# Kernel tuning notes

Hardware: AMD Instinct MI355X
Metric: run time of the kernel (lower is better)

## Reference

```python
import jax, jax.numpy as jnp
import numpy as np

N_NODES = 60000
IN_CH = 128
HID = 32
ACT_DIM = 6
N_EDGES = 600000


def setup_inputs() -> dict:
    key = jax.random.key(0)
    ks = jax.random.split(key, 10)
    state = jax.random.normal(ks[0], (N_NODES, IN_CH), dtype=jnp.float32)
    edge_index = jax.random.randint(ks[1], (2, N_EDGES), 0, N_NODES, dtype=jnp.int64)
    s_g = 1.0 / np.sqrt(IN_CH)
    s_h = 1.0 / np.sqrt(HID)
    Wg = jax.random.uniform(ks[2], (IN_CH, IN_CH), jnp.float32, -s_g, s_g)
    bg = jax.random.uniform(ks[3], (IN_CH,), jnp.float32, -s_g, s_g)
    W1 = jax.random.uniform(ks[4], (IN_CH, HID), jnp.float32, -s_g, s_g)
    b1 = jax.random.uniform(ks[5], (HID,), jnp.float32, -s_g, s_g)
    W2 = jax.random.uniform(ks[6], (HID, HID), jnp.float32, -s_h, s_h)
    b2 = jax.random.uniform(ks[7], (HID,), jnp.float32, -s_h, s_h)
    W3 = jax.random.uniform(ks[8], (HID, 1), jnp.float32, -s_h, s_h)
    b3 = jax.random.uniform(ks[9], (1,), jnp.float32, -s_h, s_h)
    return {"state": state, "Wg": Wg, "bg": bg, "W1": W1, "b1": b1,
            "W2": W2, "b2": b2, "W3": W3, "b3": b3, "edge_index": edge_index}


def reference(state, Wg, bg, W1, b1, W2, b2, W3, b3, edge_index):
    N = state.shape[0]
    # GCNConv: add self-loops, symmetric degree normalization
    loop = jnp.arange(N, dtype=edge_index.dtype)
    src = jnp.concatenate([edge_index[0], loop])
    dst = jnp.concatenate([edge_index[1], loop])
    deg = jax.ops.segment_sum(jnp.ones_like(dst, dtype=state.dtype), dst, num_segments=N)
    dinv = jax.lax.rsqrt(deg)  # deg >= 1 thanks to self-loops
    norm = dinv[src] * dinv[dst]  # [E+N]
    h = state @ Wg  # [N, C]
    agg = jax.ops.segment_sum(h[src] * norm[:, None], dst, num_segments=N) + bg
    out = jax.nn.relu(agg)
    x = (out + state).reshape(-1, ACT_DIM, IN_CH)  # [B, 6, C]
    x = jax.nn.leaky_relu(x @ W1 + b1)
    x = jax.nn.leaky_relu(x @ W2 + b2)
    conc = jax.nn.softplus(x @ W3 + b3)[..., 0]  # [B, 6]
    # deterministic, mode==0
    action = conc / (conc.sum() + 1e-20)
    return action
```

## Files before the change

### kernel.cpp

```cpp
#include <hip/hip_runtime.h>
#include <hip/hip_bf16.h>
#include <math.h>

#define N_NODES 60000
#define IN_CH   128
#define HID     32
#define N_EDGES 600000
#define CAP     48

#define WS_CNT    0
#define WS_SUM    60000
#define WS_BUCKET 60008
#define WS_HS     2940032
#define WS_X      10620032

typedef float  v4f __attribute__((ext_vector_type(4)));
typedef short  v8s __attribute__((ext_vector_type(8)));

static __device__ inline short f2bf(float f) {
    __hip_bfloat16 h = __float2bfloat16(f);
    union { __hip_bfloat16 h; short s; } u; u.h = h; return u.s;
}

__global__ void k_hist(const int* __restrict__ eidx, int* __restrict__ cnt,
                       int* __restrict__ bucket) {
    int i = blockIdx.x * blockDim.x + threadIdx.x;
    if (i >= N_EDGES) return;
    int s = eidx[i];
    int d = eidx[N_EDGES + i];
    int slot = atomicAdd(&cnt[d], 1);
    if (slot < CAP) bucket[d * CAP + slot] = s;
}

__launch_bounds__(256)
__global__ void k_gemm(const float* __restrict__ state, const float* __restrict__ Wg,
                       const int* __restrict__ cnt, unsigned short* __restrict__ hs) {
    __shared__ __align__(16) short Bs[128 * 136];
    const int t = threadIdx.x;
    for (int idx = t; idx < 128 * 128; idx += 256) {
        int k = idx >> 7, n = idx & 127;
        Bs[n * 136 + k] = f2bf(Wg[idx]);
    }
    __syncthreads();

    const int w = t >> 6, lane = t & 63;
    const int quad = lane >> 4, m = lane & 15;
    const int rowBase = blockIdx.x * 64;
    int arow = rowBase + w * 16 + m;
    if (arow > N_NODES - 1) arow = N_NODES - 1;

    v8s a[4];
    const float4* sp = (const float4*)(state + (size_t)arow * 128);
#pragma unroll
    for (int q = 0; q < 4; ++q) {
        float4 v0 = sp[q * 8 + quad * 2];
        float4 v1 = sp[q * 8 + quad * 2 + 1];
        v8s af;
        af[0] = f2bf(v0.x); af[1] = f2bf(v0.y); af[2] = f2bf(v0.z); af[3] = f2bf(v0.w);
        af[4] = f2bf(v1.x); af[5] = f2bf(v1.y); af[6] = f2bf(v1.z); af[7] = f2bf(v1.w);
        a[q] = af;
    }

    v4f acc[8];
#pragma unroll
    for (int tt = 0; tt < 8; ++tt) acc[tt] = (v4f)0.f;

#pragma unroll
    for (int tt = 0; tt < 8; ++tt) {
        const short* bp = &Bs[(tt * 16 + m) * 136];
#pragma unroll
        for (int q = 0; q < 4; ++q) {
            v8s b = *(const v8s*)(bp + q * 32 + quad * 8);
            acc[tt] = __builtin_amdgcn_mfma_f32_16x16x32_bf16(a[q], b, acc[tt], 0, 0, 0);
        }
    }

    float dinv[4];
#pragma unroll
    for (int r = 0; r < 4; ++r) {
        int rr = rowBase + w * 16 + quad * 4 + r;
        dinv[r] = (rr < N_NODES) ? rsqrtf((float)cnt[rr] + 1.0f) : 0.f;
    }
#pragma unroll
    for (int tt = 0; tt < 8; ++tt) {
#pragma unroll
        for (int r = 0; r < 4; ++r) {
            int rr = rowBase + w * 16 + quad * 4 + r;
            if (rr < N_NODES)
                hs[(size_t)rr * 128 + tt * 16 + m] = (unsigned short)f2bf(acc[tt][r] * dinv[r]);
        }
    }
}

__launch_bounds__(256)
__global__ void k_gather(const unsigned short* __restrict__ hs, const float* __restrict__ state,
                         const int* __restrict__ cnt, const int* __restrict__ bucket,
                         const float* __restrict__ bg, float* __restrict__ x) {
    const int wave = threadIdx.x >> 6, lane = threadIdx.x & 63;
    const int row = blockIdx.x * 4 + wave;
    if (row >= N_NODES) return;
    const int ci = cnt[row];
    const float dinv = rsqrtf((float)ci + 1.0f);
    const int nb = ci < CAP ? ci : CAP;

    int slot = (lane < nb) ? bucket[row * CAP + lane] : 0;

    const unsigned int* hp = (const unsigned int*)hs;
    float ax, ay;
    {
        unsigned int u = hp[row * 64 + lane];
        ax = __uint_as_float(u << 16);
        ay = __uint_as_float(u & 0xffff0000u);
    }
    int s = 0;
    for (; s + 8 <= nb; s += 8) {
        unsigned int u0 = hp[__shfl(slot, s + 0, 64) * 64 + lane];
        unsigned int u1 = hp[__shfl(slot, s + 1, 64) * 64 + lane];
        unsigned int u2 = hp[__shfl(slot, s + 2, 64) * 64 + lane];
        unsigned int u3 = hp[__shfl(slot, s + 3, 64) * 64 + lane];
        unsigned int u4 = hp[__shfl(slot, s + 4, 64) * 64 + lane];
        unsigned int u5 = hp[__shfl(slot, s + 5, 64) * 64 + lane];
        unsigned int u6 = hp[__shfl(slot, s + 6, 64) * 64 + lane];
        unsigned int u7 = hp[__shfl(slot, s + 7, 64) * 64 + lane];
        ax += __uint_as_float(u0 << 16) + __uint_as_float(u1 << 16)
            + __uint_as_float(u2 << 16) + __uint_as_float(u3 << 16)
            + __uint_as_float(u4 << 16) + __uint_as_float(u5 << 16)
            + __uint_as_float(u6 << 16) + __uint_as_float(u7 << 16);
        ay += __uint_as_float(u0 & 0xffff0000u) + __uint_as_float(u1 & 0xffff0000u)
            + __uint_as_float(u2 & 0xffff0000u) + __uint_as_float(u3 & 0xffff0000u)
            + __uint_as_float(u4 & 0xffff0000u) + __uint_as_float(u5 & 0xffff0000u)
            + __uint_as_float(u6 & 0xffff0000u) + __uint_as_float(u7 & 0xffff0000u);
    }
    for (; s + 4 <= nb; s += 4) {
        unsigned int u0 = hp[__shfl(slot, s + 0, 64) * 64 + lane];
        unsigned int u1 = hp[__shfl(slot, s + 1, 64) * 64 + lane];
        unsigned int u2 = hp[__shfl(slot, s + 2, 64) * 64 + lane];
        unsigned int u3 = hp[__shfl(slot, s + 3, 64) * 64 + lane];
        ax += __uint_as_float(u0 << 16) + __uint_as_float(u1 << 16)
            + __uint_as_float(u2 << 16) + __uint_as_float(u3 << 16);
        ay += __uint_as_float(u0 & 0xffff0000u) + __uint_as_float(u1 & 0xffff0000u)
            + __uint_as_float(u2 & 0xffff0000u) + __uint_as_float(u3 & 0xffff0000u);
    }
    for (; s < nb; ++s) {
        unsigned int u = hp[__shfl(slot, s, 64) * 64 + lane];
        ax += __uint_as_float(u << 16);
        ay += __uint_as_float(u & 0xffff0000u);
    }
    float2 bgv = ((const float2*)bg)[lane];
    float2 st  = ((const float2*)state)[row * 64 + lane];
    float2 o;
    o.x = fmaxf(fmaf(dinv, ax, bgv.x), 0.f) + st.x;
    o.y = fmaxf(fmaf(dinv, ay, bgv.y), 0.f) + st.y;
    ((float2*)x)[row * 64 + lane] = o;
}

__launch_bounds__(256)
__global__ void k_mlp(const float* __restrict__ x,
                      const float* __restrict__ W1, const float* __restrict__ b1,
                      const float* __restrict__ W2, const float* __restrict__ b2,
                      const float* __restrict__ W3, const float* __restrict__ b3,
                      float* __restrict__ out, float* __restrict__ sum) {
    __shared__ float4 W1s[128 * 8];
    __shared__ float4 W2s[32 * 8];
    __shared__ float  W3s[32];
    __shared__ float  wred[4];
    const int t = threadIdx.x;
#pragma unroll
    for (int i = 0; i < 4; ++i) W1s[t + 256 * i] = ((const float4*)W1)[t + 256 * i];
    W2s[t] = ((const float4*)W2)[t];
    if (t < 32) W3s[t] = W3[t];
    __syncthreads();

    const int r = blockIdx.x * 256 + t;
    float sp = 0.f;
    if (r < N_NODES) {
        float h1[32];
#pragma unroll
        for (int j = 0; j < 32; ++j) h1[j] = b1[j];
        const float4* xr = (const float4*)(x + (size_t)r * 128);
#pragma unroll 4
        for (int k4 = 0; k4 < 32; ++k4) {
            float4 xv = xr[k4];
            float xa[4] = {xv.x, xv.y, xv.z, xv.w};
#pragma unroll
            for (int kk = 0; kk < 4; ++kk) {
                float xk = xa[kk];
#pragma unroll
                for (int j4 = 0; j4 < 8; ++j4) {
                    float4 w = W1s[(k4 * 4 + kk) * 8 + j4];
                    h1[j4 * 4 + 0] = fmaf(xk, w.x, h1[j4 * 4 + 0]);
                    h1[j4 * 4 + 1] = fmaf(xk, w.y, h1[j4 * 4 + 1]);
                    h1[j4 * 4 + 2] = fmaf(xk, w.z, h1[j4 * 4 + 2]);
                    h1[j4 * 4 + 3] = fmaf(xk, w.w, h1[j4 * 4 + 3]);
                }
            }
        }
        float z1[32];
#pragma unroll
        for (int j = 0; j < 32; ++j) z1[j] = h1[j] > 0.f ? h1[j] : 0.01f * h1[j];
        float h2[32];
#pragma unroll
        for (int j = 0; j < 32; ++j) h2[j] = b2[j];
#pragma unroll
        for (int k = 0; k < 32; ++k) {
            float zk = z1[k];
#pragma unroll
            for (int j4 = 0; j4 < 8; ++j4) {
                float4 w = W2s[k * 8 + j4];
                h2[j4 * 4 + 0] = fmaf(zk, w.x, h2[j4 * 4 + 0]);
                h2[j4 * 4 + 1] = fmaf(zk, w.y, h2[j4 * 4 + 1]);
                h2[j4 * 4 + 2] = fmaf(zk, w.z, h2[j4 * 4 + 2]);
                h2[j4 * 4 + 3] = fmaf(zk, w.w, h2[j4 * 4 + 3]);
            }
        }
        float a3 = b3[0];
#pragma unroll
        for (int j = 0; j < 32; ++j) {
            float z2 = h2[j] > 0.f ? h2[j] : 0.01f * h2[j];
            a3 = fmaf(z2, W3s[j], a3);
        }
        sp = fmaxf(a3, 0.f) + log1pf(expf(-fabsf(a3)));
        out[r] = sp;
    }
    float p = sp;
#pragma unroll
    for (int off = 32; off >= 1; off >>= 1) p += __shfl_xor(p, off, 64);
    if ((t & 63) == 0) wred[t >> 6] = p;
    __syncthreads();
    if (t == 0) atomicAdd(sum, (wred[0] + wred[1]) + (wred[2] + wred[3]));
}

__global__ void k_norm(const float* __restrict__ sum, float* __restrict__ out) {
    int i = blockIdx.x * blockDim.x + threadIdx.x;
    if (i < N_NODES) out[i] = out[i] / (*sum + 1e-20f);
}

extern "C" void kernel_launch(void* const* d_in, const int* in_sizes, int n_in,
                              void* d_out, int out_size, void* d_ws, size_t ws_size,
                              hipStream_t stream) {
    const float* state = (const float*)d_in[0];
    const float* Wg    = (const float*)d_in[1];
    const float* bg    = (const float*)d_in[2];
    const float* W1    = (const float*)d_in[3];
    const float* b1    = (const float*)d_in[4];
    const float* W2    = (const float*)d_in[5];
    const float* b2    = (const float*)d_in[6];
    const float* W3    = (const float*)d_in[7];
    const float* b3    = (const float*)d_in[8];
    const int*   eidx  = (const int*)d_in[9];
    float* out = (float*)d_out;

    int*   wi = (int*)d_ws;
    float* wf = (float*)d_ws;
    int*   cnt    = wi + WS_CNT;
    float* sum    = wf + WS_SUM;
    int*   bucket = wi + WS_BUCKET;
    unsigned short* hs = (unsigned short*)(wf + WS_HS);
    float* x      = wf + WS_X;

    hipMemsetAsync(cnt, 0, 60001 * sizeof(int), stream);
    k_hist<<<(N_EDGES + 255) / 256, 256, 0, stream>>>(eidx, cnt, bucket);
    k_gemm<<<(N_NODES + 63) / 64, 256, 0, stream>>>(state, Wg, cnt, hs);
    k_gather<<<(N_NODES + 3) / 4, 256, 0, stream>>>(hs, state, cnt, bucket, bg, x);
    k_mlp<<<(N_NODES + 255) / 256, 256, 0, stream>>>(x, W1, b1, W2, b2, W3, b3, out, sum);
    k_norm<<<(N_NODES + 255) / 256, 256, 0, stream>>>(sum, out);
}
```

Measured before the change: 191.9 us.

## Fuse histogram and GEMM into one launch, store x as bf16

Merges the edge-bucketing histogram and the dense GEMM into one kernel whose blocks are split 2:5 between GEMM and histogram work, so both run concurrently. To remove the GEMM's dependency on degree counts, the source-side dinv scaling moves into the gather, which loads each neighbour's count and applies it per edge. The intermediate x is written as packed bf16 instead of fp32, halving its traffic into the MLP. The final normalization is vectorized to float4. This adds extra count loads and shuffles in the gather and more bf16 rounding error.

```diff
diff --git a/kernel.cpp b/kernel.cpp
--- a/kernel.cpp
+++ b/kernel.cpp
@@ -21,22 +21,32 @@
     __hip_bfloat16 h = __float2bfloat16(f);
     union { __hip_bfloat16 h; short s; } u; u.h = h; return u.s;
 }
-
-__global__ void k_hist(const int* __restrict__ eidx, int* __restrict__ cnt,
-                       int* __restrict__ bucket) {
-    int i = blockIdx.x * blockDim.x + threadIdx.x;
-    if (i >= N_EDGES) return;
-    int s = eidx[i];
-    int d = eidx[N_EDGES + i];
-    int slot = atomicAdd(&cnt[d], 1);
-    if (slot < CAP) bucket[d * CAP + slot] = s;
-}
+static __device__ inline float bflo(unsigned int u) { return __uint_as_float(u << 16); }
+static __device__ inline float bfhi(unsigned int u) { return __uint_as_float(u & 0xffff0000u); }
 
 __launch_bounds__(256)
-__global__ void k_gemm(const float* __restrict__ state, const float* __restrict__ Wg,
-                       const int* __restrict__ cnt, unsigned short* __restrict__ hs) {
+__global__ void k_fat(const float* __restrict__ state, const float* __restrict__ Wg,
+                      const int* __restrict__ eidx, int* __restrict__ cnt,
+                      int* __restrict__ bucket, unsigned short* __restrict__ hs) {
     __shared__ __align__(16) short Bs[128 * 136];
+    const int bid = blockIdx.x;
+    const int r7 = bid % 7, q7 = bid / 7;
     const int t = threadIdx.x;
+
+    if (r7 >= 2) {
+        const int hb = q7 * 5 + (r7 - 2);
+        const int i = hb * 256 + t;
+        if (i < N_EDGES) {
+            int s = eidx[i];
+            int d = eidx[N_EDGES + i];
+            int slot = atomicAdd(&cnt[d], 1);
+            if (slot < CAP) bucket[d * CAP + slot] = s;
+        }
+        return;
+    }
+
+    const int gb = q7 * 2 + r7;
+
     for (int idx = t; idx < 128 * 128; idx += 256) {
         int k = idx >> 7, n = idx & 127;
         Bs[n * 136 + k] = f2bf(Wg[idx]);
@@ -45,7 +55,7 @@
 
     const int w = t >> 6, lane = t & 63;
     const int quad = lane >> 4, m = lane & 15;
-    const int rowBase = blockIdx.x * 64;
+    const int rowBase = gb * 64;
     int arow = rowBase + w * 16 + m;
     if (arow > N_NODES - 1) arow = N_NODES - 1;
 
@@ -75,19 +85,13 @@
         }
     }
 
-    float dinv[4];
-#pragma unroll
-    for (int r = 0; r < 4; ++r) {
-        int rr = rowBase + w * 16 + quad * 4 + r;
-        dinv[r] = (rr < N_NODES) ? rsqrtf((float)cnt[rr] + 1.0f) : 0.f;
-    }
 #pragma unroll
     for (int tt = 0; tt < 8; ++tt) {
 #pragma unroll
         for (int r = 0; r < 4; ++r) {
             int rr = rowBase + w * 16 + quad * 4 + r;
             if (rr < N_NODES)
-                hs[(size_t)rr * 128 + tt * 16 + m] = (unsigned short)f2bf(acc[tt][r] * dinv[r]);
+                hs[(size_t)rr * 128 + tt * 16 + m] = (unsigned short)f2bf(acc[tt][r]);
         }
     }
 }
@@ -95,7 +99,7 @@
 __launch_bounds__(256)
 __global__ void k_gather(const unsigned short* __restrict__ hs, const float* __restrict__ state,
                          const int* __restrict__ cnt, const int* __restrict__ bucket,
-                         const float* __restrict__ bg, float* __restrict__ x) {
+                         const float* __restrict__ bg, unsigned int* __restrict__ xb) {
     const int wave = threadIdx.x >> 6, lane = threadIdx.x & 63;
     const int row = blockIdx.x * 4 + wave;
     if (row >= N_NODES) return;
@@ -103,59 +107,78 @@
     const float dinv = rsqrtf((float)ci + 1.0f);
     const int nb = ci < CAP ? ci : CAP;
 
-    int slot = (lane < nb) ? bucket[row * CAP + lane] : 0;
+    int slot = 0; float dv = 0.f;
+    if (lane < nb) {
+        slot = bucket[row * CAP + lane];
+        dv = rsqrtf((float)cnt[slot] + 1.0f);
+    }
 
     const unsigned int* hp = (const unsigned int*)hs;
     float ax, ay;
     {
-        unsigned int u = hp[row * 64 + lane];
-        ax = __uint_as_float(u << 16);
-        ay = __uint_as_float(u & 0xffff0000u);
+        unsigned int u = hp[(size_t)row * 64 + lane];
+        ax = bflo(u) * dinv;
+        ay = bfhi(u) * dinv;
     }
     int s = 0;
     for (; s + 8 <= nb; s += 8) {
-        unsigned int u0 = hp[__shfl(slot, s + 0, 64) * 64 + lane];
-        unsigned int u1 = hp[__shfl(slot, s + 1, 64) * 64 + lane];
-        unsigned int u2 = hp[__shfl(slot, s + 2, 64) * 64 + lane];
-        unsigned int u3 = hp[__shfl(slot, s + 3, 64) * 64 + lane];
-        unsigned int u4 = hp[__shfl(slot, s + 4, 64) * 64 + lane];
-        unsigned int u5 = hp[__shfl(slot, s + 5, 64) * 64 + lane];
-        unsigned int u6 = hp[__shfl(slot, s + 6, 64) * 64 + lane];
-        unsigned int u7 = hp[__shfl(slot, s + 7, 64) * 64 + lane];
-        ax += __uint_as_float(u0 << 16) + __uint_as_float(u1 << 16)
-            + __uint_as_float(u2 << 16) + __uint_as_float(u3 << 16)
-            + __uint_as_float(u4 << 16) + __uint_as_float(u5 << 16)
-            + __uint_as_float(u6 << 16) + __uint_as_float(u7 << 16);
-        ay += __uint_as_float(u0 & 0xffff0000u) + __uint_as_float(u1 & 0xffff0000u)
-            + __uint_as_float(u2 & 0xffff0000u) + __uint_as_float(u3 & 0xffff0000u)
-            + __uint_as_float(u4 & 0xffff0000u) + __uint_as_float(u5 & 0xffff0000u)
-            + __uint_as_float(u6 & 0xffff0000u) + __uint_as_float(u7 & 0xffff0000u);
+        int s0 = __shfl(slot, s + 0, 64), s1 = __shfl(slot, s + 1, 64);
+        int s2 = __shfl(slot, s + 2, 64), s3 = __shfl(slot, s + 3, 64);
+        int s4 = __shfl(slot, s + 4, 64), s5 = __shfl(slot, s + 5, 64);
+        int s6 = __shfl(slot, s + 6, 64), s7 = __shfl(slot, s + 7, 64);
+        float d0 = __shfl(dv, s + 0, 64), d1 = __shfl(dv, s + 1, 64);
+        float d2 = __shfl(dv, s + 2, 64), d3 = __shfl(dv, s + 3, 64);
+        float d4 = __shfl(dv, s + 4, 64), d5 = __shfl(dv, s + 5, 64);
+        float d6 = __shfl(dv, s + 6, 64), d7 = __shfl(dv, s + 7, 64);
+        unsigned int u0 = hp[(size_t)s0 * 64 + lane];
+        unsigned int u1 = hp[(size_t)s1 * 64 + lane];
+        unsigned int u2 = hp[(size_t)s2 * 64 + lane];
+        unsigned int u3 = hp[(size_t)s3 * 64 + lane];
+        unsigned int u4 = hp[(size_t)s4 * 64 + lane];
+        unsigned int u5 = hp[(size_t)s5 * 64 + lane];
+        unsigned int u6 = hp[(size_t)s6 * 64 + lane];
+        unsigned int u7 = hp[(size_t)s7 * 64 + lane];
+        ax = fmaf(d0, bflo(u0), ax); ay = fmaf(d0, bfhi(u0), ay);
+        ax = fmaf(d1, bflo(u1), ax); ay = fmaf(d1, bfhi(u1), ay);
+        ax = fmaf(d2, bflo(u2), ax); ay = fmaf(d2, bfhi(u2), ay);
+        ax = fmaf(d3, bflo(u3), ax); ay = fmaf(d3, bfhi(u3), ay);
+        ax = fmaf(d4, bflo(u4), ax); ay = fmaf(d4, bfhi(u4), ay);
+        ax = fmaf(d5, bflo(u5), ax); ay = fmaf(d5, bfhi(u5), ay);
+        ax = fmaf(d6, bflo(u6), ax); ay = fmaf(d6, bfhi(u6), ay);
+        ax = fmaf(d7, bflo(u7), ax); ay = fmaf(d7, bfhi(u7), ay);
     }
     for (; s + 4 <= nb; s += 4) {
-        unsigned int u0 = hp[__shfl(slot, s + 0, 64) * 64 + lane];
-        unsigned int u1 = hp[__shfl(slot, s + 1, 64) * 64 + lane];
-        unsigned int u2 = hp[__shfl(slot, s + 2, 64) * 64 + lane];
-        unsigned int u3 = hp[__shfl(slot, s + 3, 64) * 64 + lane];
-        ax += __uint_as_float(u0 << 16) + __uint_as_float(u1 << 16)
-            + __uint_as_float(u2 << 16) + __uint_as_float(u3 << 16);
-        ay += __uint_as_float(u0 & 0xffff0000u) + __uint_as_float(u1 & 0xffff0000u)
-            + __uint_as_float(u2 & 0xffff0000u) + __uint_as_float(u3 & 0xffff0000u);
+        int s0 = __shfl(slot, s + 0, 64), s1 = __shfl(slot, s + 1, 64);
+        int s2 = __shfl(slot, s + 2, 64), s3 = __shfl(slot, s + 3, 64);
+        float d0 = __shfl(dv, s + 0, 64), d1 = __shfl(dv, s + 1, 64);
+        float d2 = __shfl(dv, s + 2, 64), d3 = __shfl(dv, s + 3, 64);
+        unsigned int u0 = hp[(size_t)s0 * 64 + lane];
+        unsigned int u1 = hp[(size_t)s1 * 64 + lane];
+        unsigned int u2 = hp[(size_t)s2 * 64 + lane];
+        unsigned int u3 = hp[(size_t)s3 * 64 + lane];
+        ax = fmaf(d0, bflo(u0), ax); ay = fmaf(d0, bfhi(u0), ay);
+        ax = fmaf(d1, bflo(u1), ax); ay = fmaf(d1, bfhi(u1), ay);
+        ax = fmaf(d2, bflo(u2), ax); ay = fmaf(d2, bfhi(u2), ay);
+        ax = fmaf(d3, bflo(u3), ax); ay = fmaf(d3, bfhi(u3), ay);
     }
     for (; s < nb; ++s) {
-        unsigned int u = hp[__shfl(slot, s, 64) * 64 + lane];
-        ax += __uint_as_float(u << 16);
-        ay += __uint_as_float(u & 0xffff0000u);
+        int s0 = __shfl(slot, s, 64);
+        float d0 = __shfl(dv, s, 64);
+        unsigned int u = hp[(size_t)s0 * 64 + lane];
+        ax = fmaf(d0, bflo(u), ax);
+        ay = fmaf(d0, bfhi(u), ay);
     }
     float2 bgv = ((const float2*)bg)[lane];
-    float2 st  = ((const float2*)state)[row * 64 + lane];
-    float2 o;
-    o.x = fmaxf(fmaf(dinv, ax, bgv.x), 0.f) + st.x;
-    o.y = fmaxf(fmaf(dinv, ay, bgv.y), 0.f) + st.y;
-    ((float2*)x)[row * 64 + lane] = o;
+    float2 st  = ((const float2*)state)[(size_t)row * 64 + lane];
+    float ox = fmaxf(fmaf(dinv, ax, bgv.x), 0.f) + st.x;
+    float oy = fmaxf(fmaf(dinv, ay, bgv.y), 0.f) + st.y;
+    unsigned int pack = ((unsigned int)(unsigned short)f2bf(oy) << 16)
+                      | ((unsigned int)(unsigned short)f2bf(ox));
+    xb[(size_t)row * 64 + lane] = pack;
 }
 
 __launch_bounds__(256)
-__global__ void k_mlp(const float* __restrict__ x,
+__global__ void k_mlp(const unsigned int* __restrict__ xb,
                       const float* __restrict__ W1, const float* __restrict__ b1,
                       const float* __restrict__ W2, const float* __restrict__ b2,
                       const float* __restrict__ W3, const float* __restrict__ b3,
@@ -177,17 +200,17 @@
         float h1[32];
 #pragma unroll
         for (int j = 0; j < 32; ++j) h1[j] = b1[j];
-        const float4* xr = (const float4*)(x + (size_t)r * 128);
-#pragma unroll 4
-        for (int k4 = 0; k4 < 32; ++k4) {
-            float4 xv = xr[k4];
-            float xa[4] = {xv.x, xv.y, xv.z, xv.w};
-#pragma unroll
-            for (int kk = 0; kk < 4; ++kk) {
-                float xk = xa[kk];
+        const v8s* xr = (const v8s*)(xb + (size_t)r * 64);
+#pragma unroll 2
+        for (int k8 = 0; k8 < 16; ++k8) {
+            v8s xv = xr[k8];
+#pragma unroll
+            for (int jj = 0; jj < 8; ++jj) {
+                float xk = __uint_as_float(((unsigned int)(unsigned short)xv[jj]) << 16);
+                const int k = k8 * 8 + jj;
 #pragma unroll
                 for (int j4 = 0; j4 < 8; ++j4) {
-                    float4 w = W1s[(k4 * 4 + kk) * 8 + j4];
+                    float4 w = W1s[k * 8 + j4];
                     h1[j4 * 4 + 0] = fmaf(xk, w.x, h1[j4 * 4 + 0]);
                     h1[j4 * 4 + 1] = fmaf(xk, w.y, h1[j4 * 4 + 1]);
                     h1[j4 * 4 + 2] = fmaf(xk, w.z, h1[j4 * 4 + 2]);
@@ -232,7 +255,13 @@
 
 __global__ void k_norm(const float* __restrict__ sum, float* __restrict__ out) {
     int i = blockIdx.x * blockDim.x + threadIdx.x;
-    if (i < N_NODES) out[i] = out[i] / (*sum + 1e-20f);
+    if (i < N_NODES / 4) {
+        float inv = 1.0f / (*sum + 1e-20f);
+        float4* o4 = (float4*)out;
+        float4 v = o4[i];
+        v.x *= inv; v.y *= inv; v.z *= inv; v.w *= inv;
+        o4[i] = v;
+    }
 }
 
 extern "C" void kernel_launch(void* const* d_in, const int* in_sizes, int n_in,
@@ -256,12 +285,12 @@
     float* sum    = wf + WS_SUM;
     int*   bucket = wi + WS_BUCKET;
     unsigned short* hs = (unsigned short*)(wf + WS_HS);
-    float* x      = wf + WS_X;
+    unsigned int*   xb = (unsigned int*)(wf + WS_X);
 
     hipMemsetAsync(cnt, 0, 60001 * sizeof(int), stream);
-    k_hist<<<(N_EDGES + 255) / 256, 256, 0, stream>>>(eidx, cnt, bucket);
-    k_gemm<<<(N_NODES + 63) / 64, 256, 0, stream>>>(state, Wg, cnt, hs);
-    k_gather<<<(N_NODES + 3) / 4, 256, 0, stream>>>(hs, state, cnt, bucket, bg, x);
-    k_mlp<<<(N_NODES + 255) / 256, 256, 0, stream>>>(x, W1, b1, W2, b2, W3, b3, out, sum);
-    k_norm<<<(N_NODES + 255) / 256, 256, 0, stream>>>(sum, out);
-}
+
+    k_fat<<<3282, 256, 0, stream>>>(state, Wg, eidx, cnt, bucket, hs);
+    k_gather<<<(N_NODES + 3) / 4, 256, 0, stream>>>(hs, state, cnt, bucket, bg, xb);
+    k_mlp<<<(N_NODES + 255) / 256, 256, 0, stream>>>(xb, W1, b1, W2, b2, W3, b3, out, sum);
+    k_norm<<<(N_NODES / 4 + 255) / 256, 256, 0, stream>>>(sum, out);
+}
```

Measured after the change: 184.1 us. -4.1%, faster.
